# Kernel optimization log

Hardware: AMD Instinct MI355X
Metric: run time of the kernel (lower is better)

The kernel has to match this reference:

```python
import jax, jax.numpy as jnp
import numpy as np

EPS = 1e-6
H = 8  # number of heads


def _ln(x, a, b):
    # Custom LayerNorm from the source: uses unbiased std and divides by (std + eps)
    m = x.mean(-1, keepdims=True)
    s = x.std(-1, keepdims=True, ddof=1)
    return a * (x - m) / (s + EPS) + b


def setup_inputs() -> dict:
    key = jax.random.key(0)
    L, B, S, D, F = 6, 8, 1024, 512, 2048
    ks = jax.random.split(key, 8)
    sc = 0.02  # param init scale
    return {
        "x": jax.random.normal(ks[0], (B, S, D), jnp.float32),
        "mask": jnp.ones((B, 1, S), jnp.int32),
        "Wqkv": (jax.random.normal(ks[1], (L, 4, D, D), jnp.float32) * sc),
        "bqkv": jnp.zeros((L, 4, D), jnp.float32),
        "W1": (jax.random.normal(ks[2], (L, D, F), jnp.float32) * sc),
        "b1": jnp.zeros((L, F), jnp.float32),
        "W2": (jax.random.normal(ks[3], (L, F, D), jnp.float32) * sc),
        "b2": jnp.zeros((L, D), jnp.float32),
        "ln_a": jnp.ones((L, 2, D), jnp.float32),
        "ln_b": jnp.zeros((L, 2, D), jnp.float32),
        "fin_a": jnp.ones((D,), jnp.float32),
        "fin_b": jnp.zeros((D,), jnp.float32),
    }


def reference(x, mask, Wqkv, bqkv, W1, b1, W2, b2, ln_a, ln_b, fin_a, fin_b):
    B, S, D = x.shape
    dk = D // H
    neg_mask = (mask[:, None, :, :] == 0)  # [B,1,1,S] broadcast over heads and queries
    inv_sqrt_dk = 1.0 / jnp.sqrt(jnp.float32(dk))

    def step(h, p):
        Wq, bq, w1, bb1, w2, bb2, la, lb = p
        # --- self-attention sublayer (pre-norm + residual) ---
        y = _ln(h, la[0], lb[0])
        def proj(i):
            return (y @ Wq[i] + bq[i]).reshape(B, S, H, dk).transpose(0, 2, 1, 3)
        q, k, v = proj(0), proj(1), proj(2)
        scores = jnp.einsum('bhqd,bhkd->bhqk', q, k) * inv_sqrt_dk
        scores = jnp.where(neg_mask, jnp.float32(-1e9), scores)
        p_attn = jax.nn.softmax(scores, axis=-1)
        o = jnp.einsum('bhqk,bhkd->bhqd', p_attn, v)
        o = o.transpose(0, 2, 1, 3).reshape(B, S, D)
        h = h + (o @ Wq[3] + bq[3])
        # --- feed-forward sublayer (pre-norm + residual) ---
        y2 = _ln(h, la[1], lb[1])
        h = h + (jax.nn.relu(y2 @ w1 + bb1) @ w2 + bb2)
        return h, None

    out, _ = jax.lax.scan(step, x, (Wqkv, bqkv, W1, b1, W2, b2, ln_a, ln_b))
    return _ln(out, fin_a, fin_b)
```

## Files before the change

### kernel.cpp

```cpp
#include <hip/hip_runtime.h>
#include <stdint.h>

typedef unsigned short u16;
typedef __bf16 bf16x8 __attribute__((ext_vector_type(8)));
typedef __bf16 bf16x4v __attribute__((ext_vector_type(4)));
typedef float f32x4 __attribute__((ext_vector_type(4)));

__device__ __forceinline__ f32x4 mfma16(bf16x8 a, bf16x8 b, f32x4 c) {
  return __builtin_amdgcn_mfma_f32_16x16x32_bf16(a, b, c, 0, 0, 0);
}

__device__ __forceinline__ void gload_lds16(const void* g, void* l) {
  __builtin_amdgcn_global_load_lds((__attribute__((address_space(1))) void*)g,
                                   (__attribute__((address_space(3))) void*)l,
                                   16, 0, 0);
}

__device__ __forceinline__ u16 f2bf(float f) {
  uint32_t u = __builtin_bit_cast(uint32_t, f);
  u += 0x7fffu + ((u >> 16) & 1u);
  return (u16)(u >> 16);
}

__device__ __forceinline__ float exp2_fast(float x) {
  float r;
  asm("v_exp_f32 %0, %1" : "=v"(r) : "v"(x));
  return r;
}

__device__ __forceinline__ bf16x4v pk4(f32x4 v) {
  bf16x4v r;
  r[0] = (__bf16)v[0];
  r[1] = (__bf16)v[1];
  r[2] = (__bf16)v[2];
  r[3] = (__bf16)v[3];
  return r;
}

__global__ void transpose_cast_batch(const float* __restrict__ in,
                                     u16* __restrict__ out, int R, int C) {
  const int z = blockIdx.z;
  in += (size_t)z * R * C;
  out += (size_t)z * R * C;
  __shared__ float tile[32][33];
  const int bx = blockIdx.x * 32, by = blockIdx.y * 32;
  const int tx = threadIdx.x, ty = threadIdx.y;
  for (int i = ty; i < 32; i += 8)
    tile[i][tx] = in[(size_t)(by + i) * C + bx + tx];
  __syncthreads();
  for (int i = ty; i < 32; i += 8)
    out[(size_t)(bx + i) * R + by + tx] = f2bf(tile[tx][i]);
}

template <bool BF16OUT>
__global__ __launch_bounds__(256) void ln_rows(const float* __restrict__ in,
                                               void* __restrict__ out,
                                               const float* __restrict__ ga,
                                               const float* __restrict__ gb) {
  const int row = blockIdx.x, tid = threadIdx.x;
  const float* xr = in + (size_t)row * 512;
  const float x0 = xr[tid], x1 = xr[tid + 256];
  float s = x0 + x1;
#pragma unroll
  for (int off = 32; off > 0; off >>= 1) s += __shfl_down(s, off);
  __shared__ float red[4], red2[4];
  const int wv = tid >> 6, ln = tid & 63;
  if (ln == 0) red[wv] = s;
  __syncthreads();
  const float mean = (red[0] + red[1] + red[2] + red[3]) * (1.0f / 512.0f);
  const float d0 = x0 - mean, d1 = x1 - mean;
  float sq = d0 * d0 + d1 * d1;
#pragma unroll
  for (int off = 32; off > 0; off >>= 1) sq += __shfl_down(sq, off);
  if (ln == 0) red2[wv] = sq;
  __syncthreads();
  const float var = (red2[0] + red2[1] + red2[2] + red2[3]) * (1.0f / 511.0f);
  const float inv = 1.0f / (sqrtf(var) + 1e-6f);
  const float o0 = ga[tid] * d0 * inv + gb[tid];
  const float o1 = ga[tid + 256] * d1 * inv + gb[tid + 256];
  if constexpr (BF16OUT) {
    u16* ob = (u16*)out + (size_t)row * 512;
    ob[tid] = f2bf(o0);
    ob[tid + 256] = f2bf(o1);
  } else {
    float* of = (float*)out + (size_t)row * 512;
    of[tid] = o0;
    of[tid + 256] = o1;
  }
}

template <int EPI, bool SPLITK = false>
__global__ __launch_bounds__(256, 4) void gemm_bt(
    const u16* __restrict__ A, const u16* __restrict__ Bt,
    const float* __restrict__ bias, float* __restrict__ hres,
    u16* __restrict__ obf, u16* __restrict__ qout, u16* __restrict__ kout,
    u16* __restrict__ vout, int M, int N, int K, int kLen) {
  __shared__ __align__(16) u16 sA[128 * 64];
  __shared__ __align__(16) u16 sB[128 * 64];
  const int tid = threadIdx.x;
  const int wv = tid >> 6, ln = tid & 63;

  const int gx = gridDim.x;
  const int nwg = gx * gridDim.y;
  const int orig = blockIdx.x + gx * blockIdx.y;
  const int chunk = nwg >> 3;
  const int swz = (orig & 7) * chunk + (orig >> 3);
  const int m0 = (swz / gx) * 128, n0 = (swz % gx) * 128;

  const int kBase = SPLITK ? blockIdx.z * kLen : 0;
  const int kEnd = kBase + kLen;
  const int wr = (wv >> 1) * 64, wc = (wv & 1) * 64;
  const int l15 = ln & 15, lk8 = (ln >> 4) * 8;

  const f32x4 vzero = {0.f, 0.f, 0.f, 0.f};
  f32x4 acc[4][4];
#pragma unroll
  for (int i = 0; i < 4; ++i)
#pragma unroll
    for (int j = 0; j < 4; ++j) acc[i][j] = vzero;

#define STAGE(k0)                                                              \
  do {                                                                         \
    _Pragma("unroll") for (int it = 0; it < 4; ++it) {                         \
      const int obase = it * 4096 + wv * 1024;                                 \
      const int o = obase + (ln << 4);                                         \
      const int row = o >> 7;                                                  \
      const int scb = (o & 127) ^ ((row & 7) << 4);                            \
      gload_lds16(A + (size_t)(m0 + row) * K + (k0) + (scb >> 1),              \
                  (char*)sA + obase);                                          \
      gload_lds16(Bt + (size_t)(n0 + row) * K + (k0) + (scb >> 1),             \
                  (char*)sB + obase);                                          \
    }                                                                          \
  } while (0)

  for (int k0 = kBase; k0 < kEnd; k0 += 64) {
    STAGE(k0);
    asm volatile("s_waitcnt vmcnt(0)" ::: "memory");
    __syncthreads();
#pragma unroll
    for (int kk = 0; kk < 64; kk += 32) {
      bf16x8 af[4], bfr[4];
#pragma unroll
      for (int i = 0; i < 4; ++i) {
        const int ra = wr + i * 16 + l15;
        af[i] = *(const bf16x8*)((const char*)sA + ra * 128 +
                                 (((kk + lk8) << 1) ^ ((ra & 7) << 4)));
        const int rb = wc + i * 16 + l15;
        bfr[i] = *(const bf16x8*)((const char*)sB + rb * 128 +
                                  (((kk + lk8) << 1) ^ ((rb & 7) << 4)));
      }
#pragma unroll
      for (int i = 0; i < 4; ++i)
#pragma unroll
        for (int j = 0; j < 4; ++j) acc[i][j] = mfma16(af[i], bfr[j], acc[i][j]);
    }
    __syncthreads();
  }
#undef STAGE

#pragma unroll
  for (int i = 0; i < 4; ++i) {
    const int rowb = m0 + wr + i * 16 + ((ln >> 4) << 2);
#pragma unroll
    for (int j = 0; j < 4; ++j) {
      const int col = n0 + wc + j * 16 + l15;
      const float bs = (!SPLITK || blockIdx.z == 0) ? bias[col] : 0.f;
#pragma unroll
      for (int r = 0; r < 4; ++r) {
        const int row = rowb + r;
        const float val = acc[i][j][r] + bs;
        if constexpr (EPI == 0) {
          if constexpr (SPLITK)
            atomicAdd(&hres[(size_t)row * N + col], val);
          else
            hres[(size_t)row * N + col] += val;
        } else if constexpr (EPI == 1) {
          obf[(size_t)row * N + col] = f2bf(fmaxf(val, 0.f));
        } else {
          const int b = row >> 10, sidx = row & 1023;
          const int which = col >> 9, hn = col & 511;
          const int hh = hn >> 6, d = hn & 63;
          if (which == 0)
            qout[(((size_t)(b * 8 + hh)) * 1024 + sidx) * 64 + d] =
                f2bf(val * 0.18033688011112042f);
          else if (which == 1)
            kout[(((size_t)(b * 8 + hh)) * 1024 + sidx) * 64 + d] = f2bf(val);
          else
            vout[(((size_t)(b * 8 + hh)) * 64 + d) * 1024 + sidx] = f2bf(val);
        }
      }
    }
  }
}

__global__ __launch_bounds__(256) void attn_kernel(
    const u16* __restrict__ q, const u16* __restrict__ k,
    const u16* __restrict__ v, const int* __restrict__ mask,
    u16* __restrict__ o) {
  __shared__ __align__(16) u16 sK[2][64 * 64];
  __shared__ __align__(16) u16 sV[64 * 64];
  __shared__ __align__(16) u16 plds[4][16 * 64];
  __shared__ float sBiasF[1024];

  const int bid = blockIdx.x;
  const int xcd = bid & 7, local = bid >> 3;
  const int bh = xcd * 8 + (local >> 4), qb = local & 15;
  const int b = bh >> 3, hh = bh & 7;
  const int wv = threadIdx.x >> 6, ln = threadIdx.x & 63;
  const int q0 = qb * 64 + wv * 16;
  const u16* qb_p = q + (size_t)bh * 1024 * 64;
  const u16* kb = k + (size_t)bh * 1024 * 64;
  const u16* vb = v + (size_t)bh * 64 * 1024;
  const int* mb = mask + b * 1024;
  const int l15 = ln & 15, g = ln >> 4, g8 = g * 8, g4 = g * 4;
  const int swq = (l15 & 7) << 4;

  {
    const int4 mm = ((const int4*)mb)[threadIdx.x];
    float4 bb;
    bb.x = mm.x ? 0.f : -1e9f;
    bb.y = mm.y ? 0.f : -1e9f;
    bb.z = mm.z ? 0.f : -1e9f;
    bb.w = mm.w ? 0.f : -1e9f;
    ((float4*)sBiasF)[threadIdx.x] = bb;
  }

  bf16x8 aq[2];
  aq[0] = *(const bf16x8*)(qb_p + (size_t)(q0 + l15) * 64 + g8);
  aq[1] = *(const bf16x8*)(qb_p + (size_t)(q0 + l15) * 64 + 32 + g8);

  const f32x4 vzero = {0.f, 0.f, 0.f, 0.f};
  f32x4 accO[4] = {vzero, vzero, vzero, vzero};
  float mrun = -3.0e38f, lrun = 0.f;

#define STAGE_K(bi, t)                                                         \
  do {                                                                         \
    _Pragma("unroll") for (int it = 0; it < 2; ++it) {                         \
      const int obase = (wv * 2 + it) * 1024;                                  \
      const int oo = obase + (ln << 4);                                        \
      const int row = oo >> 7;                                                 \
      const int scb = (oo & 127) ^ ((row & 7) << 4);                           \
      gload_lds16(kb + ((size_t)((t) * 64 + row)) * 64 + (scb >> 1),           \
                  (char*)sK[bi] + obase);                                      \
    }                                                                          \
  } while (0)
#define STAGE_V(t)                                                             \
  do {                                                                         \
    _Pragma("unroll") for (int it = 0; it < 2; ++it) {                         \
      const int obase = (wv * 2 + it) * 1024;                                  \
      const int oo = obase + (ln << 4);                                        \
      const int row = oo >> 7;                                                 \
      const int scb = (oo & 127) ^ ((row & 7) << 4);                           \
      gload_lds16(vb + (size_t)row * 1024 + (t) * 64 + (scb >> 1),             \
                  (char*)sV + obase);                                          \
    }                                                                          \
  } while (0)

  STAGE_K(0, 0);
  STAGE_V(0);
  asm volatile("s_waitcnt vmcnt(0)" ::: "memory");
  __syncthreads();

  for (int t = 0; t < 16; ++t) {
    const int c = t & 1;
    if (t > 0) STAGE_V(t);
    if (t < 15) STAGE_K(c ^ 1, t + 1);
    const int kc = t * 64;

    f32x4 sc4[4];
    __builtin_amdgcn_s_setprio(1);
#pragma unroll
    for (int u = 0; u < 4; ++u) {
      const int row = u * 16 + l15;
      const char* base = (const char*)sK[c] + row * 128;
      const int sw = (row & 7) << 4;
      const bf16x8 k0 = *(const bf16x8*)(base + ((g8 << 1) ^ sw));
      const bf16x8 k1 = *(const bf16x8*)(base + ((64 + (g8 << 1)) ^ sw));
      f32x4 a = *(const f32x4*)(sBiasF + kc + u * 16 + g4);
      a = mfma16(k0, aq[0], a);
      a = mfma16(k1, aq[1], a);
      sc4[u] = a;
    }
    __builtin_amdgcn_s_setprio(0);

    float m16 = sc4[0][0];
#pragma unroll
    for (int u = 0; u < 4; ++u)
#pragma unroll
      for (int r = 0; r < 4; ++r) m16 = fmaxf(m16, sc4[u][r]);

    if (!__all(m16 <= mrun + 8.0f)) {
      float mrow = fmaxf(m16, __shfl_xor(m16, 16));
      mrow = fmaxf(mrow, __shfl_xor(mrow, 32));
      const float mnew = fmaxf(mrun, mrow);
      const float scale = exp2_fast(mrun - mnew);
      mrun = mnew;
      lrun *= scale;
#pragma unroll
      for (int f = 0; f < 4; ++f) accO[f] *= scale;
    }

    float s = 0.f;
#pragma unroll
    for (int u = 0; u < 4; ++u)
#pragma unroll
      for (int r = 0; r < 4; ++r) {
        const float p = exp2_fast(sc4[u][r] - mrun);
        sc4[u][r] = p;
        s += p;
      }
    s += __shfl_xor(s, 16);
    s += __shfl_xor(s, 32);
    lrun += s;

    char* pw = (char*)plds[wv];
#pragma unroll
    for (int u = 0; u < 4; ++u)
      *(bf16x4v*)(pw + l15 * 128 + ((u * 32 + g * 8) ^ swq)) = pk4(sc4[u]);
    const bf16x8 ap0 = *(const bf16x8*)(pw + l15 * 128 + ((g8 << 1) ^ swq));
    const bf16x8 ap1 = *(const bf16x8*)(pw + l15 * 128 + ((64 + (g8 << 1)) ^ swq));

    asm volatile("s_waitcnt vmcnt(0)" ::: "memory");

    __builtin_amdgcn_s_setprio(1);
#pragma unroll
    for (int f = 0; f < 4; ++f) {
      const int row = f * 16 + l15;
      const char* vbase = (const char*)sV + row * 128;
      const int sw2 = (row & 7) << 4;
      const bf16x8 v0 = *(const bf16x8*)(vbase + ((g8 << 1) ^ sw2));
      const bf16x8 v1 = *(const bf16x8*)(vbase + ((64 + (g8 << 1)) ^ sw2));
      accO[f] = mfma16(v0, ap0, accO[f]);
      accO[f] = mfma16(v1, ap1, accO[f]);
    }
    __builtin_amdgcn_s_setprio(0);
    __syncthreads();
  }
#undef STAGE_K
#undef STAGE_V

  const float inv = 1.0f / lrun;
  u16* orow = o + ((size_t)(b * 1024 + q0 + l15)) * 512 + hh * 64;
#pragma unroll
  for (int f = 0; f < 4; ++f)
    *(bf16x4v*)(orow + f * 16 + g4) = pk4(accO[f] * inv);
}

extern "C" void kernel_launch(void* const* d_in, const int* in_sizes, int n_in,
                              void* d_out, int out_size, void* d_ws, size_t ws_size,
                              hipStream_t stream) {
  const float* x     = (const float*)d_in[0];
  const int*   mask  = (const int*)d_in[1];
  const float* Wqkv  = (const float*)d_in[2];
  const float* bqkv  = (const float*)d_in[3];
  const float* W1    = (const float*)d_in[4];
  const float* b1    = (const float*)d_in[5];
  const float* W2    = (const float*)d_in[6];
  const float* b2    = (const float*)d_in[7];
  const float* ln_a  = (const float*)d_in[8];
  const float* ln_b  = (const float*)d_in[9];
  const float* fin_a = (const float*)d_in[10];
  const float* fin_b = (const float*)d_in[11];

  const int L = 6;
  const size_t MB = 1u << 20;
  char* ws = (char*)d_ws;
  float* h  = (float*)ws;
  u16* y    = (u16*)(ws + 16 * MB);
  u16* qbuf = (u16*)(ws + 24 * MB);
  u16* kbuf = (u16*)(ws + 32 * MB);
  u16* vbuf = (u16*)(ws + 40 * MB);
  u16* obuf = (u16*)(ws + 48 * MB);
  u16* f1   = (u16*)(ws + 24 * MB);
  u16* wqkvt = (u16*)(ws + 56 * MB);
  u16* w1t  = wqkvt + (size_t)L * 4 * 512 * 512;
  u16* w2t  = w1t + (size_t)L * 2048 * 512;

  hipMemcpyAsync(h, x, (size_t)8192 * 512 * 4, hipMemcpyDeviceToDevice, stream);

  dim3 tb(32, 8);
  transpose_cast_batch<<<dim3(16, 16, 24), tb, 0, stream>>>(Wqkv, wqkvt, 512, 512);
  transpose_cast_batch<<<dim3(64, 16, 6), tb, 0, stream>>>(W1, w1t, 512, 2048);
  transpose_cast_batch<<<dim3(16, 64, 6), tb, 0, stream>>>(W2, w2t, 2048, 512);

  for (int l = 0; l < L; ++l) {
    ln_rows<true><<<8192, 256, 0, stream>>>(h, y, ln_a + (size_t)l * 1024,
                                            ln_b + (size_t)l * 1024);
    gemm_bt<2><<<dim3(12, 64), 256, 0, stream>>>(
        y, wqkvt + (size_t)l * 4 * 512 * 512, bqkv + (size_t)l * 2048, nullptr,
        nullptr, qbuf, kbuf, vbuf, 8192, 1536, 512, 512);
    attn_kernel<<<1024, 256, 0, stream>>>(qbuf, kbuf, vbuf, mask, obuf);
    gemm_bt<0, true><<<dim3(4, 64, 2), 256, 0, stream>>>(
        obuf, wqkvt + ((size_t)l * 4 + 3) * 512 * 512,
        bqkv + (size_t)l * 2048 + 1536, h, nullptr, nullptr, nullptr, nullptr,
        8192, 512, 512, 256);
    ln_rows<true><<<8192, 256, 0, stream>>>(h, y, ln_a + (size_t)l * 1024 + 512,
                                            ln_b + (size_t)l * 1024 + 512);
    gemm_bt<1><<<dim3(16, 64), 256, 0, stream>>>(
        y, w1t + (size_t)l * 2048 * 512, b1 + (size_t)l * 2048, nullptr, f1,
        nullptr, nullptr, nullptr, 8192, 2048, 512, 512);
    gemm_bt<0, true><<<dim3(4, 64, 2), 256, 0, stream>>>(
        f1, w2t + (size_t)l * 512 * 2048, b2 + (size_t)l * 512, h, nullptr,
        nullptr, nullptr, nullptr, 8192, 512, 2048, 1024);
  }
  ln_rows<false><<<8192, 256, 0, stream>>>(h, d_out, fin_a, fin_b);
}
```

Measured before the change: 1.108 ms.

## Triple-buffer GEMM LDS pipeline with 256x128 tiles and 512-thread blocks

The bf16 GEMM now uses 256x128 output tiles computed by 8 waves per block. It keeps a three-stage ring of LDS buffers in dynamic shared memory and prefetches tile k+2 while computing tile k, waiting only on the older stage's loads via vmcnt. This removes the trailing barrier and is meant to hide global-to-LDS latency behind MFMA work. It also raises wave priority around the MFMA block. The cost is 144KB of LDS per block, so only one block fits per CU, and the grids are halved in M, which lowers occupancy and the wave count for the small-N GEMMs.

```diff
diff --git a/kernel.cpp b/kernel.cpp
--- a/kernel.cpp
+++ b/kernel.cpp
@@ -90,13 +90,12 @@
 }
 
 template <int EPI, bool SPLITK = false>
-__global__ __launch_bounds__(256, 4) void gemm_bt(
+__global__ __launch_bounds__(512, 2) void gemm_bt(
     const u16* __restrict__ A, const u16* __restrict__ Bt,
     const float* __restrict__ bias, float* __restrict__ hres,
     u16* __restrict__ obf, u16* __restrict__ qout, u16* __restrict__ kout,
     u16* __restrict__ vout, int M, int N, int K, int kLen) {
-  __shared__ __align__(16) u16 sA[128 * 64];
-  __shared__ __align__(16) u16 sB[128 * 64];
+  extern __shared__ u16 sBuf[];
   const int tid = threadIdx.x;
   const int wv = tid >> 6, ln = tid & 63;
 
@@ -105,10 +104,10 @@
   const int orig = blockIdx.x + gx * blockIdx.y;
   const int chunk = nwg >> 3;
   const int swz = (orig & 7) * chunk + (orig >> 3);
-  const int m0 = (swz / gx) * 128, n0 = (swz % gx) * 128;
+  const int m0 = (swz / gx) * 256, n0 = (swz % gx) * 128;
 
   const int kBase = SPLITK ? blockIdx.z * kLen : 0;
-  const int kEnd = kBase + kLen;
+  const int NT = kLen >> 6;
   const int wr = (wv >> 1) * 64, wc = (wv & 1) * 64;
   const int l15 = ln & 15, lk8 = (ln >> 4) * 8;
 
@@ -119,44 +118,62 @@
 #pragma unroll
     for (int j = 0; j < 4; ++j) acc[i][j] = vzero;
 
-#define STAGE(k0)                                                              \
+#define STAGE3(kt)                                                             \
   do {                                                                         \
-    _Pragma("unroll") for (int it = 0; it < 4; ++it) {                         \
-      const int obase = it * 4096 + wv * 1024;                                 \
-      const int o = obase + (ln << 4);                                         \
+    const int k0s = kBase + (kt) * 64;                                         \
+    char* dst = (char*)(sBuf + ((kt) % 3) * 24576);                            \
+    _Pragma("unroll") for (int rr = 0; rr < 4; ++rr) {                         \
+      const int o = rr * 8192 + tid * 16;                                      \
       const int row = o >> 7;                                                  \
       const int scb = (o & 127) ^ ((row & 7) << 4);                            \
-      gload_lds16(A + (size_t)(m0 + row) * K + (k0) + (scb >> 1),              \
-                  (char*)sA + obase);                                          \
-      gload_lds16(Bt + (size_t)(n0 + row) * K + (k0) + (scb >> 1),             \
-                  (char*)sB + obase);                                          \
+      gload_lds16(A + (size_t)(m0 + row) * K + k0s + (scb >> 1),               \
+                  dst + rr * 8192 + wv * 1024);                                \
+    }                                                                          \
+    _Pragma("unroll") for (int rr = 0; rr < 2; ++rr) {                         \
+      const int o = rr * 8192 + tid * 16;                                      \
+      const int row = o >> 7;                                                  \
+      const int scb = (o & 127) ^ ((row & 7) << 4);                            \
+      gload_lds16(Bt + (size_t)(n0 + row) * K + k0s + (scb >> 1),              \
+                  dst + 32768 + rr * 8192 + wv * 1024);                        \
     }                                                                          \
   } while (0)
 
-  for (int k0 = kBase; k0 < kEnd; k0 += 64) {
-    STAGE(k0);
-    asm volatile("s_waitcnt vmcnt(0)" ::: "memory");
+  STAGE3(0);
+  if (NT > 1) STAGE3(1);
+
+  for (int kt = 0; kt < NT; ++kt) {
+    if (kt + 1 < NT)
+      asm volatile("s_waitcnt vmcnt(6)" ::: "memory");
+    else
+      asm volatile("s_waitcnt vmcnt(0)" ::: "memory");
     __syncthreads();
+
+    const u16* pA = sBuf + (kt % 3) * 24576;
+    const u16* pB = pA + 16384;
+
+    if (kt + 2 < NT) STAGE3(kt + 2);
+
 #pragma unroll
     for (int kk = 0; kk < 64; kk += 32) {
       bf16x8 af[4], bfr[4];
 #pragma unroll
       for (int i = 0; i < 4; ++i) {
         const int ra = wr + i * 16 + l15;
-        af[i] = *(const bf16x8*)((const char*)sA + ra * 128 +
+        af[i] = *(const bf16x8*)((const char*)pA + ra * 128 +
                                  (((kk + lk8) << 1) ^ ((ra & 7) << 4)));
         const int rb = wc + i * 16 + l15;
-        bfr[i] = *(const bf16x8*)((const char*)sB + rb * 128 +
+        bfr[i] = *(const bf16x8*)((const char*)pB + rb * 128 +
                                   (((kk + lk8) << 1) ^ ((rb & 7) << 4)));
       }
+      __builtin_amdgcn_s_setprio(1);
 #pragma unroll
       for (int i = 0; i < 4; ++i)
 #pragma unroll
         for (int j = 0; j < 4; ++j) acc[i][j] = mfma16(af[i], bfr[j], acc[i][j]);
+      __builtin_amdgcn_s_setprio(0);
     }
-    __syncthreads();
-  }
-#undef STAGE
+  }
+#undef STAGE3
 
 #pragma unroll
   for (int i = 0; i < 4; ++i) {
@@ -364,6 +381,7 @@
 
   const int L = 6;
   const size_t MB = 1u << 20;
+  const int GEMM_LDS = 147456;
   char* ws = (char*)d_ws;
   float* h  = (float*)ws;
   u16* y    = (u16*)(ws + 16 * MB);
@@ -376,6 +394,13 @@
   u16* w1t  = wqkvt + (size_t)L * 4 * 512 * 512;
   u16* w2t  = w1t + (size_t)L * 2048 * 512;
 
+  hipFuncSetAttribute((const void*)gemm_bt<2, false>,
+                      hipFuncAttributeMaxDynamicSharedMemorySize, GEMM_LDS);
+  hipFuncSetAttribute((const void*)gemm_bt<0, true>,
+                      hipFuncAttributeMaxDynamicSharedMemorySize, GEMM_LDS);
+  hipFuncSetAttribute((const void*)gemm_bt<1, false>,
+                      hipFuncAttributeMaxDynamicSharedMemorySize, GEMM_LDS);
+
   hipMemcpyAsync(h, x, (size_t)8192 * 512 * 4, hipMemcpyDeviceToDevice, stream);
 
   dim3 tb(32, 8);
@@ -386,20 +411,20 @@
   for (int l = 0; l < L; ++l) {
     ln_rows<true><<<8192, 256, 0, stream>>>(h, y, ln_a + (size_t)l * 1024,
                                             ln_b + (size_t)l * 1024);
-    gemm_bt<2><<<dim3(12, 64), 256, 0, stream>>>(
+    gemm_bt<2><<<dim3(12, 32), 512, GEMM_LDS, stream>>>(
         y, wqkvt + (size_t)l * 4 * 512 * 512, bqkv + (size_t)l * 2048, nullptr,
         nullptr, qbuf, kbuf, vbuf, 8192, 1536, 512, 512);
     attn_kernel<<<1024, 256, 0, stream>>>(qbuf, kbuf, vbuf, mask, obuf);
-    gemm_bt<0, true><<<dim3(4, 64, 2), 256, 0, stream>>>(
+    gemm_bt<0, true><<<dim3(4, 32, 2), 512, GEMM_LDS, stream>>>(
         obuf, wqkvt + ((size_t)l * 4 + 3) * 512 * 512,
         bqkv + (size_t)l * 2048 + 1536, h, nullptr, nullptr, nullptr, nullptr,
         8192, 512, 512, 256);
     ln_rows<true><<<8192, 256, 0, stream>>>(h, y, ln_a + (size_t)l * 1024 + 512,
                                             ln_b + (size_t)l * 1024 + 512);
-    gemm_bt<1><<<dim3(16, 64), 256, 0, stream>>>(
+    gemm_bt<1><<<dim3(16, 32), 512, GEMM_LDS, stream>>>(
         y, w1t + (size_t)l * 2048 * 512, b1 + (size_t)l * 2048, nullptr, f1,
         nullptr, nullptr, nullptr, 8192, 2048, 512, 512);
-    gemm_bt<0, true><<<dim3(4, 64, 2), 256, 0, stream>>>(
+    gemm_bt<0, true><<<dim3(4, 32, 2), 512, GEMM_LDS, stream>>>(
         f1, w2t + (size_t)l * 512 * 2048, b2 + (size_t)l * 512, h, nullptr,
         nullptr, nullptr, nullptr, 8192, 512, 2048, 1024);
   }
```

After: 1.178 ms. +6.3%, slower.

## Load GEMM fragments directly from global into registers, drop LDS staging

Applied to the files above, without the earlier changes.

The GEMM kernel no longer stages A/B tiles through shared memory with global_load_lds and barriers. Each wave now loads its MFMA operand fragments straight from global memory into registers, double-buffered across 32-wide K halves, and raises wave priority around MFMA bursts. Launch bounds drop to 3 waves per SIMD to make room for the extra registers. This removes LDS traffic and block syncs, but loses cross-wave data sharing: each tile is fetched from global/L2 by multiple waves, and the loads are strided 16-byte row reads rather than coalesced.

```diff
diff --git a/kernel.cpp b/kernel.cpp
--- a/kernel.cpp
+++ b/kernel.cpp
@@ -90,13 +90,11 @@
 }
 
 template <int EPI, bool SPLITK = false>
-__global__ __launch_bounds__(256, 4) void gemm_bt(
+__global__ __launch_bounds__(256, 3) void gemm_bt(
     const u16* __restrict__ A, const u16* __restrict__ Bt,
     const float* __restrict__ bias, float* __restrict__ hres,
     u16* __restrict__ obf, u16* __restrict__ qout, u16* __restrict__ kout,
     u16* __restrict__ vout, int M, int N, int K, int kLen) {
-  __shared__ __align__(16) u16 sA[128 * 64];
-  __shared__ __align__(16) u16 sB[128 * 64];
   const int tid = threadIdx.x;
   const int wv = tid >> 6, ln = tid & 63;
 
@@ -108,10 +106,17 @@
   const int m0 = (swz / gx) * 128, n0 = (swz % gx) * 128;
 
   const int kBase = SPLITK ? blockIdx.z * kLen : 0;
-  const int kEnd = kBase + kLen;
   const int wr = (wv >> 1) * 64, wc = (wv & 1) * 64;
   const int l15 = ln & 15, lk8 = (ln >> 4) * 8;
 
+  const u16* pa[4];
+  const u16* pb[4];
+#pragma unroll
+  for (int i = 0; i < 4; ++i) {
+    pa[i] = A + (size_t)(m0 + wr + i * 16 + l15) * K + kBase + lk8;
+    pb[i] = Bt + (size_t)(n0 + wc + i * 16 + l15) * K + kBase + lk8;
+  }
+
   const f32x4 vzero = {0.f, 0.f, 0.f, 0.f};
   f32x4 acc[4][4];
 #pragma unroll
@@ -119,44 +124,39 @@
 #pragma unroll
     for (int j = 0; j < 4; ++j) acc[i][j] = vzero;
 
-#define STAGE(k0)                                                              \
+#define LOADH(av, bv, koff)                                                    \
   do {                                                                         \
-    _Pragma("unroll") for (int it = 0; it < 4; ++it) {                         \
-      const int obase = it * 4096 + wv * 1024;                                 \
-      const int o = obase + (ln << 4);                                         \
-      const int row = o >> 7;                                                  \
-      const int scb = (o & 127) ^ ((row & 7) << 4);                            \
-      gload_lds16(A + (size_t)(m0 + row) * K + (k0) + (scb >> 1),              \
-                  (char*)sA + obase);                                          \
-      gload_lds16(Bt + (size_t)(n0 + row) * K + (k0) + (scb >> 1),             \
-                  (char*)sB + obase);                                          \
+    _Pragma("unroll") for (int i = 0; i < 4; ++i) {                            \
+      av[i] = *(const bf16x8*)(pa[i] + (koff));                                \
+      bv[i] = *(const bf16x8*)(pb[i] + (koff));                                \
     }                                                                          \
   } while (0)
 
-  for (int k0 = kBase; k0 < kEnd; k0 += 64) {
-    STAGE(k0);
-    asm volatile("s_waitcnt vmcnt(0)" ::: "memory");
-    __syncthreads();
-#pragma unroll
-    for (int kk = 0; kk < 64; kk += 32) {
-      bf16x8 af[4], bfr[4];
-#pragma unroll
-      for (int i = 0; i < 4; ++i) {
-        const int ra = wr + i * 16 + l15;
-        af[i] = *(const bf16x8*)((const char*)sA + ra * 128 +
-                                 (((kk + lk8) << 1) ^ ((ra & 7) << 4)));
-        const int rb = wc + i * 16 + l15;
-        bfr[i] = *(const bf16x8*)((const char*)sB + rb * 128 +
-                                  (((kk + lk8) << 1) ^ ((rb & 7) << 4)));
-      }
-#pragma unroll
-      for (int i = 0; i < 4; ++i)
-#pragma unroll
-        for (int j = 0; j < 4; ++j) acc[i][j] = mfma16(af[i], bfr[j], acc[i][j]);
+#define MFMA16(av, bv)                                                         \
+  do {                                                                         \
+    __builtin_amdgcn_s_setprio(1);                                             \
+    _Pragma("unroll") for (int i = 0; i < 4; ++i)                              \
+        _Pragma("unroll") for (int j = 0; j < 4; ++j)                          \
+            acc[i][j] = mfma16(av[i], bv[j], acc[i][j]);                       \
+    __builtin_amdgcn_s_setprio(0);                                             \
+  } while (0)
+
+  const int NH = kLen >> 5;
+  bf16x8 a0[4], b0[4], a1[4], b1[4];
+  LOADH(a0, b0, 0);
+  int ko = 32;
+  for (int kh = 0; kh + 2 <= NH; kh += 2) {
+    LOADH(a1, b1, ko);
+    ko += 32;
+    MFMA16(a0, b0);
+    if (kh + 2 < NH) {
+      LOADH(a0, b0, ko);
+      ko += 32;
     }
-    __syncthreads();
-  }
-#undef STAGE
+    MFMA16(a1, b1);
+  }
+#undef LOADH
+#undef MFMA16
 
 #pragma unroll
   for (int i = 0; i < 4; ++i) {
```

Measured after the change: 1.713 ms. +54.6%, slower.
